# Kernel tuning notes

Hardware: AMD Instinct MI355X
Metric: run time of the kernel (lower is better)

The kernel has to match this reference:

```python
import jax, jax.numpy as jnp
import numpy as np

B, N, H, NH, M = 4, 8192, 1024, 16, 64
D = H // NH  # head_dim = 64
SCALE = D ** -0.5


def setup_inputs() -> dict:
    key = jax.random.key(0)
    ks = jax.random.split(key, 10)
    inp = {
        'x': jax.random.normal(ks[0], (B, N, H), jnp.float32),
        'c': jax.random.normal(ks[1], (B, H), jnp.float32),
        'w_kv': jax.random.normal(ks[2], (H, 2 * H), jnp.float32) * (H ** -0.5),
        'b_kv': jnp.zeros((2 * H,), jnp.float32),
        'w_temp': jax.random.normal(ks[3], (H, NH), jnp.float32) * (H ** -0.5),
        'b_temp': jnp.zeros((NH,), jnp.float32),
        'xq': jax.random.normal(ks[4], (NH, M, D), jnp.float32) * (D ** -0.5),
        'qkv_proj': jax.random.normal(ks[5], (NH, D, 3 * D), jnp.float32) * 0.02,
        'w_out': jax.random.normal(ks[6], (H, H), jnp.float32) * (H ** -0.5),
        'b_out': jnp.zeros((H,), jnp.float32),
    }
    return inp


def reference(x, c, w_kv, b_kv, w_temp, b_temp, xq, qkv_proj, w_out, b_out):
    b, n, h = x.shape
    # kv slice projections -> [b, h, n, d]
    kv = x @ w_kv + b_kv
    xk, xv = jnp.split(kv, 2, axis=-1)
    xk = xk.reshape(b, n, NH, D).transpose(0, 2, 1, 3)
    xv = xv.reshape(b, n, NH, D).transpose(0, 2, 1, 3)
    # per-token learned temperature: [b, n, heads] -> [b, heads, 1, n]
    temperature = 0.5 + jax.nn.softplus(x @ w_temp + b_temp)
    temperature = temperature.transpose(0, 2, 1)[:, :, None, :]
    # slice scores and softmax over SLICE (query) dim m
    slice_scores = jnp.einsum('hmd,bhnd->bhmn', xq, xk)
    slice_weights = jax.nn.softmax(slice_scores / temperature, axis=-2)
    slice_norm = slice_weights.sum(axis=-1)  # [b, h, m]
    slice_token = jnp.einsum('bhmn,bhnd->bhmd', slice_weights, xv)
    slice_token = slice_token / (slice_norm[..., None] + 1e-5)
    # tiny intra-slice 'attention' (faithfully elementwise, softmax over d)
    qkv = jnp.einsum('bhmd,hde->bhme', slice_token, qkv_proj)
    q_t, k_t, v_t = jnp.split(qkv, 3, axis=-1)
    dots = q_t * k_t * SCALE          # einsum 'bhqd,bhdq->bhqd' == elementwise
    attn = jax.nn.softmax(dots, axis=-1)
    out_slice_token = attn * v_t       # einsum 'bhqd,bhqd->bhqd' == elementwise
    # scatter back to tokens via slice_weights
    out_x = jnp.einsum('bhmd,bhmn->bhnd', out_slice_token, slice_weights)
    out_x = out_x.transpose(0, 2, 1, 3).reshape(b, n, h)
    return out_x @ w_out + b_out
```

## Files before the change

### kernel.cpp

```cpp
#include <hip/hip_runtime.h>
#include <hip/hip_bf16.h>


#define NTOK 32768
#define HH   1024
#define NHD  16
#define DD   64

typedef short short8 __attribute__((ext_vector_type(8)));
typedef float f32x4 __attribute__((ext_vector_type(4)));

#define AS1 __attribute__((address_space(1)))
#define AS3 __attribute__((address_space(3)))

__device__ __forceinline__ void glds16(const void* g, void* l) {
  __builtin_amdgcn_global_load_lds((const AS1 void*)g, (AS3 void*)l, 16, 0, 0);
}

__device__ __forceinline__ void split1(float v, __hip_bfloat16& h, __hip_bfloat16& l) {
  h = __float2bfloat16(v);
  l = __float2bfloat16(v - __bfloat162float(h));
}


__global__ __launch_bounds__(256) void k_acat_t(const float* __restrict__ w_kv,
                                                const float* __restrict__ xq,
                                                __hip_bfloat16* __restrict__ wbth,
                                                __hip_bfloat16* __restrict__ wbtl) {
  int hd = blockIdx.x >> 3, kt = blockIdx.x & 7, k0 = kt * 128;
  __shared__ float xqs[64 * 65];
  __shared__ float wks[128 * 65];
  int t = threadIdx.x;
  for (int j = 0; j < 16; ++j) {
    int idx = t + 256 * j; int m = idx >> 6, d = idx & 63;
    xqs[m * 65 + d] = xq[hd * 4096 + idx];
  }
  for (int j = 0; j < 32; ++j) {
    int idx = t + 256 * j; int r = idx >> 6, c = idx & 63;
    wks[r * 65 + c] = w_kv[(size_t)(k0 + r) * 2048 + hd * 64 + c];
  }
  __syncthreads();
  int m = t & 63, kg = t >> 6;
  __hip_bfloat16 hbuf[32], lbuf[32];
  for (int i = 0; i < 32; ++i) {
    int k = kg * 32 + i;
    float s = 0.f;
    #pragma unroll 8
    for (int d = 0; d < 64; ++d) s = fmaf(wks[k * 65 + d], xqs[m * 65 + d], s);
    split1(s, hbuf[i], lbuf[i]);
  }
  size_t o = (size_t)(hd * 64 + m) * 1024 + k0 + kg * 32;
  for (int i = 0; i < 32; i += 8) {
    *(uint4*)&wbth[o + i] = *(uint4*)&hbuf[i];
    *(uint4*)&wbtl[o + i] = *(uint4*)&lbuf[i];
  }
}

__global__ __launch_bounds__(256) void k_tsplit(const float* __restrict__ src, int ld,
                                                __hip_bfloat16* __restrict__ dh,
                                                __hip_bfloat16* __restrict__ dl) {
  __shared__ float tile[64 * 65];
  int br = blockIdx.y * 64, bc = blockIdx.x * 64;
  int t = threadIdx.x;
  for (int j = 0; j < 16; ++j) {
    int idx = t + 256 * j; int r = idx >> 6, c = idx & 63;
    tile[r * 65 + c] = src[(size_t)(br + r) * ld + bc + c];
  }
  __syncthreads();
  for (int j = 0; j < 16; ++j) {
    int idx = t + 256 * j; int c = idx >> 6, r = idx & 63;
    float v = tile[r * 65 + c];
    __hip_bfloat16 hv, lv; split1(v, hv, lv);
    size_t o = (size_t)(bc + c) * 1024 + br + r;
    dh[o] = hv; dl[o] = lv;
  }
}

__global__ void k_split(const float* __restrict__ src, __hip_bfloat16* __restrict__ hi,
                        __hip_bfloat16* __restrict__ lo) {
  size_t base = ((size_t)blockIdx.x * 256 + threadIdx.x) * 8;
  float4 v0 = *(const float4*)&src[base];
  float4 v1 = *(const float4*)&src[base + 4];
  float vv[8] = {v0.x, v0.y, v0.z, v0.w, v1.x, v1.y, v1.z, v1.w};
  __hip_bfloat16 h8[8], l8[8];
  #pragma unroll
  for (int i = 0; i < 8; ++i) split1(vv[i], h8[i], l8[i]);
  *(uint4*)&hi[base] = *(uint4*)h8;
  *(uint4*)&lo[base] = *(uint4*)l8;
}

__global__ __launch_bounds__(512, 2) void k_mfma8(
    const __hip_bfloat16* __restrict__ Ah, const __hip_bfloat16* __restrict__ Al,
    const __hip_bfloat16* __restrict__ Bh, const __hip_bfloat16* __restrict__ Bl,
    const float* __restrict__ bias, float* __restrict__ C, int ldc) {
  __shared__ __align__(16) char lds[131072];
  const int t = threadIdx.x;
  const int w = t >> 6, lane = t & 63;

  const int gx = gridDim.x;
  const int nwg = gx * gridDim.y;
  const int bid = blockIdx.y * gx + blockIdx.x;
  const int swzb = (bid & 7) * (nwg >> 3) + (bid >> 3);
  const int n0 = (swzb % gx) * 256;
  const int m0 = (swzb / gx) * 256;

  const int wr = w >> 2, wc = w & 3;
  const int fm = lane & 15, kq = lane >> 4;

  int offA[8], offB[4];
  #pragma unroll
  for (int i = 0; i < 8; ++i) {
    int row = wr * 128 + i * 16 + fm;
    offA[i] = (row >> 1) * 128 + ((((row & 1) << 2) | kq) ^ ((row >> 1) & 7)) * 16;
  }
  #pragma unroll
  for (int j = 0; j < 4; ++j) {
    int row = wc * 64 + j * 16 + fm;
    offB[j] = (row >> 1) * 128 + ((((row & 1) << 2) | kq) ^ ((row >> 1) & 7)) * 16;
  }

  const int sp = lane >> 3, su = (lane & 7) ^ sp;
  const int srow = 2 * sp + (su >> 2);
  const int scol = (su & 3) * 8;
  const int aO0 = (m0 + w * 16 + srow) * 1024 + scol;
  const int aO1 = aO0 + 128 * 1024;
  const int bO0 = (n0 + w * 16 + srow) * 1024 + scol;
  const int bO1 = bO0 + 128 * 1024;
  const int ldst = w * 1024 + lane * 16;

  f32x4 acc[8][4];
  #pragma unroll
  for (int i = 0; i < 8; ++i)
    #pragma unroll
    for (int j = 0; j < 4; ++j) acc[i][j] = (f32x4){0.f, 0.f, 0.f, 0.f};

  auto stage = [&](int ts) {
    int koff = (ts >> 1) * 32;
    char* buf = &lds[(ts & 3) * 32768];
    const __hip_bfloat16* As = (ts & 1) ? Al : Ah;
    const __hip_bfloat16* Bs = (ts & 1) ? Bl : Bh;
    glds16(As + aO0 + koff, buf + ldst);
    glds16(As + aO1 + koff, buf + 8192 + ldst);
    glds16(Bs + bO0 + koff, buf + 16384 + ldst);
    glds16(Bs + bO1 + koff, buf + 24576 + ldst);
  };

  stage(0); stage(1); stage(2);
  asm volatile("s_waitcnt vmcnt(8)" ::: "memory");
  __builtin_amdgcn_s_barrier();
  __builtin_amdgcn_sched_barrier(0);

  short8 ah[8], bh[4], xb[4];
  for (int k = 0; k < 32; ++k) {
    const int v0 = 2 * k, v1 = v0 + 1;
    const char* rb0 = &lds[(v0 & 3) * 32768];
    const char* rb1 = &lds[(v1 & 3) * 32768];

    int ts0 = v0 + 3; if (ts0 > 63) ts0 = 63;
    stage(ts0);
    #pragma unroll
    for (int i = 0; i < 8; ++i) ah[i] = *(const short8*)(rb0 + offA[i]);
    #pragma unroll
    for (int j = 0; j < 4; ++j) bh[j] = *(const short8*)(rb0 + 16384 + offB[j]);
    __builtin_amdgcn_s_setprio(1);
    #pragma unroll
    for (int i = 0; i < 8; ++i)
      #pragma unroll
      for (int j = 0; j < 4; ++j)
        acc[i][j] = __builtin_amdgcn_mfma_f32_16x16x32_bf16(ah[i], bh[j], acc[i][j], 0, 0, 0);
    __builtin_amdgcn_s_setprio(0);
    asm volatile("s_waitcnt vmcnt(8)" ::: "memory");
    __builtin_amdgcn_s_barrier();
    __builtin_amdgcn_sched_barrier(0);

    int ts1 = v1 + 3; if (ts1 > 63) ts1 = 63;
    stage(ts1);
    #pragma unroll
    for (int j = 0; j < 4; ++j) xb[j] = *(const short8*)(rb1 + 16384 + offB[j]);
    __builtin_amdgcn_s_setprio(1);
    #pragma unroll
    for (int i = 0; i < 8; ++i)
      #pragma unroll
      for (int j = 0; j < 4; ++j)
        acc[i][j] = __builtin_amdgcn_mfma_f32_16x16x32_bf16(ah[i], xb[j], acc[i][j], 0, 0, 0);
    __builtin_amdgcn_s_setprio(0);
    #pragma unroll
    for (int i = 0; i < 8; ++i) ah[i] = *(const short8*)(rb1 + offA[i]);
    __builtin_amdgcn_s_setprio(1);
    #pragma unroll
    for (int i = 0; i < 8; ++i)
      #pragma unroll
      for (int j = 0; j < 4; ++j)
        acc[i][j] = __builtin_amdgcn_mfma_f32_16x16x32_bf16(ah[i], bh[j], acc[i][j], 0, 0, 0);
    __builtin_amdgcn_s_setprio(0);
    asm volatile("s_waitcnt vmcnt(8)" ::: "memory");
    __builtin_amdgcn_s_barrier();
    __builtin_amdgcn_sched_barrier(0);
  }

  asm volatile("s_waitcnt vmcnt(0)" ::: "memory");
  __builtin_amdgcn_sched_barrier(0);

  const int cm = (lane >> 4) * 4, cn = lane & 15;
  #pragma unroll
  for (int j = 0; j < 4; ++j) {
    int col = n0 + wc * 64 + j * 16 + cn;
    float bbv = bias[col];
    #pragma unroll
    for (int i = 0; i < 8; ++i) {
      int row = m0 + wr * 128 + i * 16 + cm;
      f32x4 v = acc[i][j];
      #pragma unroll
      for (int r = 0; r < 4; ++r)
        C[(size_t)(row + r) * ldc + col] = v[r] + bbv;
    }
  }
}

__global__ __launch_bounds__(256) void k_acat(const float* __restrict__ w_kv,
                                              const float* __restrict__ xq,
                                              float* __restrict__ wbig) {
  int h = blockIdx.x >> 3, kt = blockIdx.x & 7, k0 = kt * 128;
  __shared__ float xqs[64 * 68];
  __shared__ float wks[128 * 68];
  int t = threadIdx.x;
  for (int j = 0; j < 16; ++j) {
    int idx = t + 256 * j; int m = idx >> 6, d = idx & 63;
    xqs[m * 68 + d] = xq[h * 4096 + idx];
  }
  for (int j = 0; j < 32; ++j) {
    int idx = t + 256 * j; int r = idx >> 6, c = idx & 63;
    wks[r * 68 + c] = w_kv[(k0 + r) * 2048 + h * 64 + c];
  }
  __syncthreads();
  int k = t >> 1, half = t & 1;
  float out[32];
  for (int mi = 0; mi < 32; ++mi) {
    int m = half * 32 + mi;
    float s = 0.f;
    #pragma unroll 8
    for (int d = 0; d < 64; ++d) s = fmaf(wks[k * 68 + d], xqs[m * 68 + d], s);
    out[mi] = s;
  }
  float* dst = &wbig[(k0 + k) * 2048 + h * 64 + half * 32];
  for (int mi = 0; mi < 32; mi += 4)
    *(float4*)(dst + mi) = make_float4(out[mi], out[mi + 1], out[mi + 2], out[mi + 3]);
}

__global__ void k_copyv(const float* __restrict__ w_kv, float* __restrict__ wbig) {
  int idx4 = blockIdx.x * 256 + threadIdx.x;
  int k = idx4 >> 8, j4 = idx4 & 255;
  int off = k * 2048 + 1024 + j4 * 4;
  *(float4*)(wbig + off) = *(const float4*)(w_kv + off);
}

__global__ void k_bias1(const float* __restrict__ xq, const float* __restrict__ b_kv,
                        float* __restrict__ bias1) {
  int j = blockIdx.x * 256 + threadIdx.x;
  if (j < 1024) {
    int h = j >> 6, m = j & 63;
    float s = 0.f;
    for (int d = 0; d < 64; ++d) s = fmaf(xq[h * 4096 + m * 64 + d], b_kv[h * 64 + d], s);
    bias1[j] = s;
  } else {
    bias1[j] = b_kv[j];
  }
}

__global__ __launch_bounds__(256) void k_temp(const float* __restrict__ x,
                                              const float* __restrict__ w_temp,
                                              const float* __restrict__ b_temp,
                                              float* __restrict__ T) {
  __shared__ float xs[16 * 1028];
  int t = threadIdx.x;
  int bn0 = blockIdx.x * 16;
  for (int j = 0; j < 16; ++j) {
    int idx4 = t + 256 * j; int row = idx4 >> 8, c4 = (idx4 & 255) * 4;
    *(float4*)&xs[row * 1028 + c4] = *(const float4*)&x[(bn0 + row) * 1024 + c4];
  }
  __syncthreads();
  int tok = t >> 4, j = t & 15;
  float z = b_temp[j];
  for (int k = 0; k < 1024; ++k) z = fmaf(xs[tok * 1028 + k], w_temp[k * 16 + j], z);
  float sp = fmaxf(z, 0.f) + log1pf(expf(-fabsf(z)));
  T[(bn0 + tok) * 16 + j] = 0.5f + sp;
}

__global__ __launch_bounds__(256) void k_gemm(const float* __restrict__ A, int lda,
                                              const float* __restrict__ Bm, int ldb,
                                              const float* __restrict__ bias,
                                              float* __restrict__ C, int ldc, int K) {
  __shared__ float As[8 * 132];
  __shared__ float Bs[8 * 132];
  int t = threadIdx.x;
  int m0 = blockIdx.y * 128, n0 = blockIdx.x * 128;
  int ar = t >> 1, ac = (t & 1) * 4;
  int bk = t >> 5, bc = (t & 31) * 4;
  const float* Ag = A + (size_t)(m0 + ar) * lda + ac;
  const float* Bg = Bm + (size_t)bk * ldb + n0 + bc;
  int tx = t & 15, ty = t >> 4;
  float acc[8][8] = {};
  float4 a4 = *(const float4*)Ag;
  float4 b4 = *(const float4*)Bg;
  for (int kt = 0; kt < K; kt += 8) {
    __syncthreads();
    As[(ac + 0) * 132 + ar] = a4.x;
    As[(ac + 1) * 132 + ar] = a4.y;
    As[(ac + 2) * 132 + ar] = a4.z;
    As[(ac + 3) * 132 + ar] = a4.w;
    *(float4*)&Bs[bk * 132 + bc] = b4;
    __syncthreads();
    if (kt + 8 < K) {
      a4 = *(const float4*)(Ag + kt + 8);
      b4 = *(const float4*)(Bg + (size_t)(kt + 8) * ldb);
    }
    #pragma unroll
    for (int k = 0; k < 8; ++k) {
      float av[8], bv[8];
      *(float4*)&av[0] = *(float4*)&As[k * 132 + ty * 8];
      *(float4*)&av[4] = *(float4*)&As[k * 132 + ty * 8 + 4];
      *(float4*)&bv[0] = *(float4*)&Bs[k * 132 + tx * 4];
      *(float4*)&bv[4] = *(float4*)&Bs[k * 132 + 64 + tx * 4];
      #pragma unroll
      for (int i = 0; i < 8; ++i)
        #pragma unroll
        for (int j = 0; j < 8; ++j) acc[i][j] = fmaf(av[i], bv[j], acc[i][j]);
    }
  }
  float4 bb0 = *(const float4*)&bias[n0 + tx * 4];
  float4 bb1 = *(const float4*)&bias[n0 + 64 + tx * 4];
  #pragma unroll
  for (int i = 0; i < 8; ++i) {
    float* crow = C + (size_t)(m0 + ty * 8 + i) * ldc + n0;
    float4 o0 = make_float4(acc[i][0] + bb0.x, acc[i][1] + bb0.y,
                            acc[i][2] + bb0.z, acc[i][3] + bb0.w);
    float4 o1 = make_float4(acc[i][4] + bb1.x, acc[i][5] + bb1.y,
                            acc[i][6] + bb1.z, acc[i][7] + bb1.w);
    *(float4*)&crow[tx * 4] = o0;
    *(float4*)&crow[64 + tx * 4] = o1;
  }
}

__global__ __launch_bounds__(256) void k_smax(float* __restrict__ S, const float* __restrict__ T,
                                              float* __restrict__ token, float* __restrict__ norm) {
  int pair = blockIdx.x >> 3, chunk = blockIdx.x & 7;
  int b = pair >> 4, h = pair & 15;
  __shared__ float sm[128 * 68];
  __shared__ float xv[128 * 68];
  int t = threadIdx.x;
  int m = t >> 2, dg = t & 3;
  float acc[16] = {};
  float nacc = 0.f;
  for (int s = 0; s < 8; ++s) {
    int bn0 = b * 8192 + chunk * 1024 + s * 128;
    for (int jj = 0; jj < 8; ++jj) {
      int idx4 = t + 256 * jj; int row = idx4 >> 4, c4 = (idx4 & 15) * 4;
      int g = (bn0 + row) * 2048 + h * 64 + c4;
      *(float4*)&sm[row * 68 + c4] = *(const float4*)&S[g];
      *(float4*)&xv[row * 68 + c4] = *(const float4*)&S[g + 1024];
    }
    __syncthreads();
    if (t < 128) {
      float tt = T[(bn0 + t) * 16 + h];
      float inv = 1.f / tt;
      float* row = &sm[t * 68];
      float mx = -1e30f;
      for (int mm = 0; mm < 64; ++mm) mx = fmaxf(mx, row[mm]);
      float sum = 0.f;
      for (int mm = 0; mm < 64; ++mm) { float e = expf((row[mm] - mx) * inv); row[mm] = e; sum += e; }
      float sinv = 1.f / sum;
      for (int mm = 0; mm < 64; ++mm) row[mm] *= sinv;
    }
    __syncthreads();
    for (int jj = 0; jj < 8; ++jj) {
      int idx4 = t + 256 * jj; int row = idx4 >> 4, c4 = (idx4 & 15) * 4;
      int g = (bn0 + row) * 2048 + h * 64 + c4;
      *(float4*)&S[g] = *(const float4*)&sm[row * 68 + c4];
    }
    for (int n = 0; n < 128; ++n) {
      float w = sm[n * 68 + m];
      if (dg == 0) nacc += w;
      const float* xr = &xv[n * 68 + dg * 16];
      #pragma unroll
      for (int q = 0; q < 4; ++q) {
        float4 v = *(const float4*)&xr[q * 4];
        acc[q * 4 + 0] = fmaf(w, v.x, acc[q * 4 + 0]);
        acc[q * 4 + 1] = fmaf(w, v.y, acc[q * 4 + 1]);
        acc[q * 4 + 2] = fmaf(w, v.z, acc[q * 4 + 2]);
        acc[q * 4 + 3] = fmaf(w, v.w, acc[q * 4 + 3]);
      }
    }
    __syncthreads();
  }
  int tb = pair * 4096 + m * 64 + dg * 16;
  for (int q = 0; q < 16; ++q) atomicAdd(&token[tb + q], acc[q]);
  if (dg == 0) atomicAdd(&norm[pair * 64 + m], nacc);
}

__global__ __launch_bounds__(256) void k_stagec(const float* __restrict__ token,
                                                const float* __restrict__ norm,
                                                const float* __restrict__ proj,
                                                float* __restrict__ ost) {
  int pair = blockIdx.x; int h = pair & 15;
  __shared__ float st[64 * 68];
  __shared__ float qk[64 * 196];
  int t = threadIdx.x;
  for (int j = 0; j < 16; ++j) {
    int idx = t + 256 * j; int m = idx >> 6, d = idx & 63;
    st[m * 68 + d] = token[pair * 4096 + idx] / (norm[pair * 64 + m] + 1e-5f);
  }
  __syncthreads();
  for (int idx = t; idx < 64 * 192; idx += 256) {
    int m = idx / 192, e = idx % 192;
    float s = 0.f;
    const float* pr = &proj[h * 12288 + e];
    const float* sr = &st[m * 68];
    for (int d = 0; d < 64; ++d) s = fmaf(sr[d], pr[d * 192], s);
    qk[m * 196 + e] = s;
  }
  __syncthreads();
  if (t < 64) {
    const float* q = &qk[t * 196];
    float dots[64];
    float mx = -1e30f;
    for (int d = 0; d < 64; ++d) { dots[d] = q[d] * q[64 + d] * 0.125f; mx = fmaxf(mx, dots[d]); }
    float sum = 0.f;
    for (int d = 0; d < 64; ++d) { dots[d] = expf(dots[d] - mx); sum += dots[d]; }
    float sinv = 1.f / sum;
    for (int d = 0; d < 64; ++d) ost[pair * 4096 + t * 64 + d] = dots[d] * sinv * q[128 + d];
  }
}

__global__ __launch_bounds__(256) void k_staged(float* __restrict__ S, const float* __restrict__ ost) {
  int pair = blockIdx.x >> 6, chunk = blockIdx.x & 63;
  int b = pair >> 4, h = pair & 15;
  __shared__ float ws[128 * 68];
  int t = threadIdx.x;
  int bn0 = b * 8192 + chunk * 128;
  for (int jj = 0; jj < 8; ++jj) {
    int idx4 = t + 256 * jj; int row = idx4 >> 4, c4 = (idx4 & 15) * 4;
    *(float4*)&ws[row * 68 + c4] = *(const float4*)&S[(bn0 + row) * 2048 + h * 64 + c4];
  }
  int d = t & 63, ng = t >> 6;
  float o[64];
  #pragma unroll
  for (int mm = 0; mm < 64; ++mm) o[mm] = ost[pair * 4096 + mm * 64 + d];
  __syncthreads();
  for (int i = 0; i < 32; ++i) {
    int n = ng + 4 * i;
    const float* wr = &ws[n * 68];
    float s = 0.f;
    #pragma unroll
    for (int mm = 0; mm < 64; ++mm) s = fmaf(wr[mm], o[mm], s);
    S[(bn0 + n) * 2048 + 1024 + h * 64 + d] = s;
  }
}

__global__ __launch_bounds__(256) void k_staged_bf(const float* __restrict__ S,
                                                   const float* __restrict__ ost,
                                                   __hip_bfloat16* __restrict__ oxh,
                                                   __hip_bfloat16* __restrict__ oxl) {
  int pair = blockIdx.x >> 6, chunk = blockIdx.x & 63;
  int b = pair >> 4, hd = pair & 15;
  __shared__ float ws[128 * 68];
  int t = threadIdx.x;
  int bn0 = b * 8192 + chunk * 128;
  for (int jj = 0; jj < 8; ++jj) {
    int idx4 = t + 256 * jj; int row = idx4 >> 4, c4 = (idx4 & 15) * 4;
    *(float4*)&ws[row * 68 + c4] = *(const float4*)&S[(bn0 + row) * 2048 + hd * 64 + c4];
  }
  int d = t & 63, ng = t >> 6;
  float o[64];
  #pragma unroll
  for (int mm = 0; mm < 64; ++mm) o[mm] = ost[pair * 4096 + mm * 64 + d];
  __syncthreads();
  for (int i = 0; i < 32; ++i) {
    int n = ng + 4 * i;
    const float* wr = &ws[n * 68];
    float s = 0.f;
    #pragma unroll
    for (int mm = 0; mm < 64; ++mm) s = fmaf(wr[mm], o[mm], s);
    __hip_bfloat16 hv, lv; split1(s, hv, lv);
    size_t oo = (size_t)(bn0 + n) * 1024 + hd * 64 + d;
    oxh[oo] = hv; oxl[oo] = lv;
  }
}

extern "C" void kernel_launch(void* const* d_in, const int* in_sizes, int n_in,
                              void* d_out, int out_size, void* d_ws, size_t ws_size,
                              hipStream_t stream) {
  const float* x      = (const float*)d_in[0];
  const float* w_kv   = (const float*)d_in[2];
  const float* b_kv   = (const float*)d_in[3];
  const float* w_temp = (const float*)d_in[4];
  const float* b_temp = (const float*)d_in[5];
  const float* xq     = (const float*)d_in[6];
  const float* proj   = (const float*)d_in[7];
  const float* w_out  = (const float*)d_in[8];
  const float* b_out  = (const float*)d_in[9];
  float* out = (float*)d_out;

  float* ws    = (float*)d_ws;
  float* S     = ws;
  float* T     = S + 67108864;
  float* BIAS1 = T + 524288;
  float* TOKEN = BIAS1 + 2048;
  float* NORM  = TOKEN + 262144;
  float* OST   = NORM + 4096;
  float* FEND  = OST + 262144;
  __hip_bfloat16* WbTh = (__hip_bfloat16*)FEND;
  __hip_bfloat16* WbTl = WbTh + 2097152;
  __hip_bfloat16* WoTh = WbTl + 2097152;
  __hip_bfloat16* WoTl = WoTh + 1048576;
  __hip_bfloat16* XH   = WoTl + 1048576;
  __hip_bfloat16* XL   = XH + 33554432;
  const size_t need_fast = 419454976ULL;

  hipMemsetAsync(TOKEN, 0, (262144 + 4096) * sizeof(float), stream);
  k_bias1<<<8, 256, 0, stream>>>(xq, b_kv, BIAS1);
  k_temp<<<2048, 256, 0, stream>>>(x, w_temp, b_temp, T);

  if (ws_size >= need_fast) {
    k_acat_t<<<128, 256, 0, stream>>>(w_kv, xq, WbTh, WbTl);
    k_tsplit<<<dim3(16, 16), 256, 0, stream>>>(w_kv + 1024, 2048,
                                               WbTh + 1048576, WbTl + 1048576);
    k_tsplit<<<dim3(16, 16), 256, 0, stream>>>(w_out, 1024, WoTh, WoTl);
    k_split<<<16384, 256, 0, stream>>>(x, XH, XL);
    k_mfma8<<<dim3(8, 128), 512, 0, stream>>>(XH, XL, WbTh, WbTl, BIAS1, S, 2048);
    k_smax<<<512, 256, 0, stream>>>(S, T, TOKEN, NORM);
    k_stagec<<<64, 256, 0, stream>>>(TOKEN, NORM, proj, OST);
    k_staged_bf<<<4096, 256, 0, stream>>>(S, OST, XH, XL);
    k_mfma8<<<dim3(4, 128), 512, 0, stream>>>(XH, XL, WoTh, WoTl, b_out, out, 1024);
  } else {
    float* WBIG = (float*)WbTh;
    k_acat<<<128, 256, 0, stream>>>(w_kv, xq, WBIG);
    k_copyv<<<1024, 256, 0, stream>>>(w_kv, WBIG);
    k_gemm<<<dim3(16, 256), 256, 0, stream>>>(x, 1024, WBIG, 2048, BIAS1, S, 2048, 1024);
    k_smax<<<512, 256, 0, stream>>>(S, T, TOKEN, NORM);
    k_stagec<<<64, 256, 0, stream>>>(TOKEN, NORM, proj, OST);
    k_staged<<<4096, 256, 0, stream>>>(S, OST);
    k_gemm<<<dim3(8, 256), 256, 0, stream>>>(S + 1024, 2048, w_out, 1024, b_out, out, 1024, 1024);
  }
}
```

Measured before the change: 1.417 ms.

## Read V and slice weights directly from global memory, reorder MFMA LDS reads

In the softmax/token-accumulation kernel, the V tile is no longer staged in shared memory. Threads are remapped so each wave shares one d-group and reads V rows straight from global memory (wave-uniform broadcast loads). The scatter-back kernel drops its LDS staging of slice weights and reads weight rows from global with wave-uniform float4 loads, using four partial accumulators. The GEMM main loop issues its LDS fragment reads before the next async global-to-LDS stage. Together these cut LDS footprint and barriers, at the cost of relying on cache hits for repeated global reads.

```diff
diff --git a/kernel.cpp b/kernel.cpp
--- a/kernel.cpp
+++ b/kernel.cpp
@@ -157,11 +157,11 @@
     const char* rb1 = &lds[(v1 & 3) * 32768];
 
     int ts0 = v0 + 3; if (ts0 > 63) ts0 = 63;
+    #pragma unroll
+    for (int j = 0; j < 4; ++j) bh[j] = *(const short8*)(rb0 + 16384 + offB[j]);
+    #pragma unroll
+    for (int i = 0; i < 8; ++i) ah[i] = *(const short8*)(rb0 + offA[i]);
     stage(ts0);
-    #pragma unroll
-    for (int i = 0; i < 8; ++i) ah[i] = *(const short8*)(rb0 + offA[i]);
-    #pragma unroll
-    for (int j = 0; j < 4; ++j) bh[j] = *(const short8*)(rb0 + 16384 + offB[j]);
     __builtin_amdgcn_s_setprio(1);
     #pragma unroll
     for (int i = 0; i < 8; ++i)
@@ -174,9 +174,9 @@
     __builtin_amdgcn_sched_barrier(0);
 
     int ts1 = v1 + 3; if (ts1 > 63) ts1 = 63;
+    #pragma unroll
+    for (int j = 0; j < 4; ++j) xb[j] = *(const short8*)(rb1 + 16384 + offB[j]);
     stage(ts1);
-    #pragma unroll
-    for (int j = 0; j < 4; ++j) xb[j] = *(const short8*)(rb1 + 16384 + offB[j]);
     __builtin_amdgcn_s_setprio(1);
     #pragma unroll
     for (int i = 0; i < 8; ++i)
@@ -341,23 +341,23 @@
   }
 }
 
-__global__ __launch_bounds__(256) void k_smax(float* __restrict__ S, const float* __restrict__ T,
+__global__ __launch_bounds__(256) void k_smax(float* __restrict__ S,
+                                              const float* __restrict__ SX,
+                                              const float* __restrict__ T,
                                               float* __restrict__ token, float* __restrict__ norm) {
   int pair = blockIdx.x >> 3, chunk = blockIdx.x & 7;
   int b = pair >> 4, h = pair & 15;
   __shared__ float sm[128 * 68];
-  __shared__ float xv[128 * 68];
-  int t = threadIdx.x;
-  int m = t >> 2, dg = t & 3;
+  int t = threadIdx.x;
+  int m = t & 63, dg = t >> 6;
   float acc[16] = {};
   float nacc = 0.f;
   for (int s = 0; s < 8; ++s) {
     int bn0 = b * 8192 + chunk * 1024 + s * 128;
     for (int jj = 0; jj < 8; ++jj) {
       int idx4 = t + 256 * jj; int row = idx4 >> 4, c4 = (idx4 & 15) * 4;
-      int g = (bn0 + row) * 2048 + h * 64 + c4;
-      *(float4*)&sm[row * 68 + c4] = *(const float4*)&S[g];
-      *(float4*)&xv[row * 68 + c4] = *(const float4*)&S[g + 1024];
+      *(float4*)&sm[row * 68 + c4] =
+          *(const float4*)&S[(size_t)(bn0 + row) * 2048 + h * 64 + c4];
     }
     __syncthreads();
     if (t < 128) {
@@ -374,21 +374,22 @@
     __syncthreads();
     for (int jj = 0; jj < 8; ++jj) {
       int idx4 = t + 256 * jj; int row = idx4 >> 4, c4 = (idx4 & 15) * 4;
-      int g = (bn0 + row) * 2048 + h * 64 + c4;
-      *(float4*)&S[g] = *(const float4*)&sm[row * 68 + c4];
+      *(float4*)&S[(size_t)(bn0 + row) * 2048 + h * 64 + c4] =
+          *(const float4*)&sm[row * 68 + c4];
     }
     for (int n = 0; n < 128; ++n) {
       float w = sm[n * 68 + m];
       if (dg == 0) nacc += w;
-      const float* xr = &xv[n * 68 + dg * 16];
-      #pragma unroll
-      for (int q = 0; q < 4; ++q) {
-        float4 v = *(const float4*)&xr[q * 4];
-        acc[q * 4 + 0] = fmaf(w, v.x, acc[q * 4 + 0]);
-        acc[q * 4 + 1] = fmaf(w, v.y, acc[q * 4 + 1]);
-        acc[q * 4 + 2] = fmaf(w, v.z, acc[q * 4 + 2]);
-        acc[q * 4 + 3] = fmaf(w, v.w, acc[q * 4 + 3]);
-      }
+      const float4* xr = (const float4*)&SX[(size_t)(bn0 + n) * 2048 + h * 64 + dg * 16];
+      float4 v0 = xr[0], v1 = xr[1], v2 = xr[2], v3 = xr[3];
+      acc[0]  = fmaf(w, v0.x, acc[0]);  acc[1]  = fmaf(w, v0.y, acc[1]);
+      acc[2]  = fmaf(w, v0.z, acc[2]);  acc[3]  = fmaf(w, v0.w, acc[3]);
+      acc[4]  = fmaf(w, v1.x, acc[4]);  acc[5]  = fmaf(w, v1.y, acc[5]);
+      acc[6]  = fmaf(w, v1.z, acc[6]);  acc[7]  = fmaf(w, v1.w, acc[7]);
+      acc[8]  = fmaf(w, v2.x, acc[8]);  acc[9]  = fmaf(w, v2.y, acc[9]);
+      acc[10] = fmaf(w, v2.z, acc[10]); acc[11] = fmaf(w, v2.w, acc[11]);
+      acc[12] = fmaf(w, v3.x, acc[12]); acc[13] = fmaf(w, v3.y, acc[13]);
+      acc[14] = fmaf(w, v3.z, acc[14]); acc[15] = fmaf(w, v3.w, acc[15]);
     }
     __syncthreads();
   }
@@ -462,25 +463,26 @@
                                                    __hip_bfloat16* __restrict__ oxl) {
   int pair = blockIdx.x >> 6, chunk = blockIdx.x & 63;
   int b = pair >> 4, hd = pair & 15;
-  __shared__ float ws[128 * 68];
-  int t = threadIdx.x;
+  int t = threadIdx.x;
+  int wave = t >> 6, d = t & 63;
   int bn0 = b * 8192 + chunk * 128;
-  for (int jj = 0; jj < 8; ++jj) {
-    int idx4 = t + 256 * jj; int row = idx4 >> 4, c4 = (idx4 & 15) * 4;
-    *(float4*)&ws[row * 68 + c4] = *(const float4*)&S[(bn0 + row) * 2048 + hd * 64 + c4];
-  }
-  int d = t & 63, ng = t >> 6;
   float o[64];
   #pragma unroll
   for (int mm = 0; mm < 64; ++mm) o[mm] = ost[pair * 4096 + mm * 64 + d];
-  __syncthreads();
   for (int i = 0; i < 32; ++i) {
-    int n = ng + 4 * i;
-    const float* wr = &ws[n * 68];
-    float s = 0.f;
-    #pragma unroll
-    for (int mm = 0; mm < 64; ++mm) s = fmaf(wr[mm], o[mm], s);
-    __hip_bfloat16 hv, lv; split1(s, hv, lv);
+    int n = wave * 32 + i;
+    const float4* wrow = (const float4*)&S[(size_t)(bn0 + n) * 2048 + hd * 64];
+    float a0 = 0.f, a1 = 0.f, a2 = 0.f, a3 = 0.f;
+    #pragma unroll
+    for (int mq = 0; mq < 16; ++mq) {
+      float4 wv = wrow[mq];
+      a0 = fmaf(wv.x, o[mq * 4 + 0], a0);
+      a1 = fmaf(wv.y, o[mq * 4 + 1], a1);
+      a2 = fmaf(wv.z, o[mq * 4 + 2], a2);
+      a3 = fmaf(wv.w, o[mq * 4 + 3], a3);
+    }
+    float sres = (a0 + a1) + (a2 + a3);
+    __hip_bfloat16 hv, lv; split1(sres, hv, lv);
     size_t oo = (size_t)(bn0 + n) * 1024 + hd * 64 + d;
     oxh[oo] = hv; oxl[oo] = lv;
   }
@@ -527,7 +529,7 @@
     k_tsplit<<<dim3(16, 16), 256, 0, stream>>>(w_out, 1024, WoTh, WoTl);
     k_split<<<16384, 256, 0, stream>>>(x, XH, XL);
     k_mfma8<<<dim3(8, 128), 512, 0, stream>>>(XH, XL, WbTh, WbTl, BIAS1, S, 2048);
-    k_smax<<<512, 256, 0, stream>>>(S, T, TOKEN, NORM);
+    k_smax<<<512, 256, 0, stream>>>(S, S + 1024, T, TOKEN, NORM);
     k_stagec<<<64, 256, 0, stream>>>(TOKEN, NORM, proj, OST);
     k_staged_bf<<<4096, 256, 0, stream>>>(S, OST, XH, XL);
     k_mfma8<<<dim3(4, 128), 512, 0, stream>>>(XH, XL, WoTh, WoTl, b_out, out, 1024);
@@ -536,7 +538,7 @@
     k_acat<<<128, 256, 0, stream>>>(w_kv, xq, WBIG);
     k_copyv<<<1024, 256, 0, stream>>>(w_kv, WBIG);
     k_gemm<<<dim3(16, 256), 256, 0, stream>>>(x, 1024, WBIG, 2048, BIAS1, S, 2048, 1024);
-    k_smax<<<512, 256, 0, stream>>>(S, T, TOKEN, NORM);
+    k_smax<<<512, 256, 0, stream>>>(S, S + 1024, T, TOKEN, NORM);
     k_stagec<<<64, 256, 0, stream>>>(TOKEN, NORM, proj, OST);
     k_staged<<<4096, 256, 0, stream>>>(S, OST);
     k_gemm<<<dim3(8, 256), 256, 0, stream>>>(S + 1024, 2048, w_out, 1024, b_out, out, 1024, 1024);
```

Measured after the change: 1.821 ms. 1.29x slower.
